# Performance work log

Measured on AMD Instinct MI355X. Metric: run time of the kernel, lower is better.

## Reference

```python
import jax, jax.numpy as jnp
import numpy as np

K = 16          # neighbors
LEAKY = 0.2     # LeakyReLU negative slope
EPS = 1e-5      # BatchNorm eps


def _edge_feature(x, k):
    # x: (B, C, N) -> edge features (B, 2C, N, k)
    xt = jnp.swapaxes(x, 1, 2)                      # (B, N, C)
    sq = jnp.sum(xt * xt, axis=-1)                  # (B, N)
    inner = jnp.einsum('bnc,bmc->bnm', xt, xt)      # (B, N, N)
    # negative squared distance (larger = closer), matches torch topk of -dist
    pd = 2.0 * inner - sq[:, :, None] - sq[:, None, :]
    _, idx = jax.lax.top_k(pd, k)                   # (B, N, k) int32
    # gather neighbors: neigh[b,n,j,c] = xt[b, idx[b,n,j], c]
    neigh = jnp.take_along_axis(xt[:, None, :, :], idx[:, :, :, None], axis=2)  # (B,N,k,C)
    center = jnp.broadcast_to(xt[:, :, None, :], neigh.shape)
    ef = jnp.concatenate([center, neigh - center], axis=-1)  # (B, N, k, 2C)
    return jnp.transpose(ef, (0, 3, 1, 2))                   # (B, 2C, N, k)


def _conv_bn_lrelu_relu(ef, W, gamma, beta):
    # 1x1 conv (no bias) + BatchNorm2d (training-mode batch stats) + LeakyReLU + ReLU
    y = jnp.einsum('oc,bcnk->bonk', W, ef)          # (B, O, N, k)
    mean = jnp.mean(y, axis=(0, 2, 3), keepdims=True)
    var = jnp.mean(jnp.square(y - mean), axis=(0, 2, 3), keepdims=True)
    y = (y - mean) * jax.lax.rsqrt(var + EPS)
    y = gamma[None, :, None, None] * y + beta[None, :, None, None]
    y = jnp.where(y > 0, y, LEAKY * y)              # LeakyReLU(0.2)
    return jax.nn.relu(y)                           # outer F.relu in forward


def setup_inputs() -> dict:
    key = jax.random.key(0)
    ks = jax.random.split(key, 12)
    B, C, N = 8, 3, 4096
    d = {
        'x':   jax.random.normal(ks[0], (B, C, N), jnp.float32),
        'W1':  jax.random.normal(ks[1], (32, 6), jnp.float32) * (1.0 / np.sqrt(6)),
        'g1':  jnp.ones((32,), jnp.float32),
        'b1':  jnp.zeros((32,), jnp.float32),
        'W2':  jax.random.normal(ks[2], (32, 64), jnp.float32) * (1.0 / np.sqrt(64)),
        'g2':  jnp.ones((32,), jnp.float32),
        'b2':  jnp.zeros((32,), jnp.float32),
        'W3':  jax.random.normal(ks[3], (64, 64), jnp.float32) * (1.0 / np.sqrt(64)),
        'g3':  jnp.ones((64,), jnp.float32),
        'b3':  jnp.zeros((64,), jnp.float32),
        'Wfc': jax.random.normal(ks[4], (64, 128), jnp.float32) * (1.0 / np.sqrt(128)),
        'bfc': jnp.zeros((64,), jnp.float32),
    }
    return d


def reference(x, W1, g1, b1, W2, g2, b2, W3, g3, b3, Wfc, bfc):
    x1 = jnp.max(_conv_bn_lrelu_relu(_edge_feature(x,  K), W1, g1, b1), axis=-1)  # (B,32,N)
    x2 = jnp.max(_conv_bn_lrelu_relu(_edge_feature(x1, K), W2, g2, b2), axis=-1)  # (B,32,N)
    x3 = jnp.max(_conv_bn_lrelu_relu(_edge_feature(x2, K), W3, g3, b3), axis=-1)  # (B,64,N)
    x_cat = jnp.concatenate([x1, x2, x3], axis=1)   # (B, 128, N)
    x_global = jnp.max(x_cat, axis=-1)              # (B, 128)
    return x_global @ Wfc.T + bfc                   # (B, 64)
```

## Files before the change

kernel.cpp:

```cpp
#include <hip/hip_runtime.h>

constexpr int B_ = 8;
constexpr int N_ = 4096;
constexpr int BN_ = B_ * N_;
constexpr float BN_EPS = 1e-5f;
constexpr int NCH_ = 8;

__global__ void prep0_kernel(const float* __restrict__ x, float* __restrict__ xa0) {
  int i = blockIdx.x * 256 + threadIdx.x;
  int b = i >> 12, n = i & (N_ - 1);
  const float* xb = x + (size_t)b * 3 * N_;
  float x0 = xb[n], x1 = xb[N_ + n], x2 = xb[2 * N_ + n];
  float4 v = make_float4(x0, x1, x2, -0.5f * (x0 * x0 + x1 * x1 + x2 * x2));
  *reinterpret_cast<float4*>(xa0 + (size_t)i * 4) = v;
}

__device__ __forceinline__ float min16f(const float tv[16]) {
  float m0 = fminf(tv[0], tv[1]),   m1 = fminf(tv[2], tv[3]);
  float m2 = fminf(tv[4], tv[5]),   m3 = fminf(tv[6], tv[7]);
  float m4 = fminf(tv[8], tv[9]),   m5 = fminf(tv[10], tv[11]);
  float m6 = fminf(tv[12], tv[13]), m7 = fminf(tv[14], tv[15]);
  return fminf(fminf(fminf(m0, m1), fminf(m2, m3)), fminf(fminf(m4, m5), fminf(m6, m7)));
}

__device__ __forceinline__ void replace16(float tv[16], int ti[16], float d, int idx,
                                          float& curmin) {
  unsigned mp = __float_as_uint(curmin);
  unsigned s = mp & 15u;
  float dp = __uint_as_float((__float_as_uint(d) & ~15u) | s);
#pragma unroll
  for (int k = 0; k < 16; ++k) {
    bool hit = (__float_as_uint(tv[k]) == mp);
    tv[k] = hit ? dp : tv[k];
    ti[k] = hit ? idx : ti[k];
  }
  curmin = min16f(tv);
}

template<int CQ>
__global__ __launch_bounds__(256, 4) void knn_kernel(const float* __restrict__ xa,
                                                     float2* __restrict__ cand16) {
  constexpr int STR = CQ * 4;
  constexpr int NF = (CQ == 1) ? 3 : 32;
  constexpr int TILE = 128;
  constexpr int CHUNK = 4096 / NCH_;
  constexpr int NT = CHUNK / TILE;
  constexpr int TILE_F = TILE * STR;
  constexpr int NPRE = (TILE_F / 4 + 255) / 256;
  __shared__ float tile[2][TILE_F];

  const int b = blockIdx.y;
  const int chunk = blockIdx.x & (NCH_ - 1);
  const int rg = blockIdx.x / NCH_;
  const int row = rg * 256 + threadIdx.x;
  const float* base = xa + (size_t)b * N_ * STR;

  float rf[NF];
  if constexpr (CQ == 1) {
    float4 v = *reinterpret_cast<const float4*>(base + (size_t)row * STR);
    rf[0] = v.x; rf[1] = v.y; rf[2] = v.z;
  } else {
#pragma unroll
    for (int q = 0; q < 8; ++q) {
      float4 v = *reinterpret_cast<const float4*>(base + (size_t)row * STR + 4 * q);
      rf[4 * q] = v.x; rf[4 * q + 1] = v.y; rf[4 * q + 2] = v.z; rf[4 * q + 3] = v.w;
    }
  }

  float tv[16]; int ti[16];
#pragma unroll
  for (int i = 0; i < 16; ++i) {
    tv[i] = __uint_as_float((__float_as_uint(-3.0e38f) & ~15u) | (unsigned)i);
    ti[i] = 0;
  }
  float curmin = min16f(tv);

  const int m0 = chunk * CHUNK;

  {
    const float4* src = reinterpret_cast<const float4*>(base + (size_t)m0 * STR);
    float4* dst = reinterpret_cast<float4*>(tile[0]);
    for (int f = threadIdx.x; f < TILE_F / 4; f += 256) dst[f] = src[f];
  }
  __syncthreads();

  for (int t = 0; t < NT; ++t) {
    const int cur = t & 1;
    float4 pre[NPRE];
    const bool hasNext = (t + 1 < NT);
    if (hasNext) {
      const float4* src = reinterpret_cast<const float4*>(base + (size_t)(m0 + (t + 1) * TILE) * STR);
#pragma unroll
      for (int k = 0; k < NPRE; ++k) {
        int f = threadIdx.x + k * 256;
        if (f < TILE_F / 4) pre[k] = src[f];
      }
    }
    const float* tl = tile[cur];
    for (int mb = 0; mb < TILE; mb += 8) {
      float d[8];
#pragma unroll
      for (int q8 = 0; q8 < 8; ++q8) {
        const float* cf = tl + (mb + q8) * STR;
        float a;
        if constexpr (CQ == 1) {
          float4 v = *reinterpret_cast<const float4*>(cf);
          a = v.w;
          a = fmaf(rf[0], v.x, a);
          a = fmaf(rf[1], v.y, a);
          a = fmaf(rf[2], v.z, a);
        } else {
          a = cf[32];
#pragma unroll
          for (int q = 0; q < 8; ++q) {
            float4 v = reinterpret_cast<const float4*>(cf)[q];
            a = fmaf(rf[4 * q], v.x, a);
            a = fmaf(rf[4 * q + 1], v.y, a);
            a = fmaf(rf[4 * q + 2], v.z, a);
            a = fmaf(rf[4 * q + 3], v.w, a);
          }
        }
        d[q8] = a;
      }
      float mx = d[0];
#pragma unroll
      for (int q8 = 1; q8 < 8; ++q8) mx = fmaxf(mx, d[q8]);
      const int mbase = m0 + t * TILE + mb;
      if (mx > curmin) {
#pragma unroll
        for (int q8 = 0; q8 < 8; ++q8)
          if (d[q8] > curmin) replace16(tv, ti, d[q8], mbase + q8, curmin);
      }
    }
    if (hasNext) {
      float4* dst = reinterpret_cast<float4*>(tile[cur ^ 1]);
#pragma unroll
      for (int k = 0; k < NPRE; ++k) {
        int f = threadIdx.x + k * 256;
        if (f < TILE_F / 4) dst[f] = pre[k];
      }
    }
    __syncthreads();
  }

  float2* outp = cand16 + ((size_t)(chunk * B_ + b) * N_ + row) * 16;
#pragma unroll
  for (int i = 0; i < 16; ++i)
    outp[i] = make_float2(tv[i], __int_as_float(ti[i]));
}

__global__ void knn_merge_kernel(const float2* __restrict__ cand16, int* __restrict__ idx_out) {
  const int i = blockIdx.x * 256 + threadIdx.x;
  float tv[16]; int ti[16];
  const float2* c0 = cand16 + (size_t)i * 16;
#pragma unroll
  for (int k = 0; k < 16; ++k) { float2 pr = c0[k]; tv[k] = pr.x; ti[k] = __float_as_int(pr.y); }
  float curmin = min16f(tv);
  for (int c = 1; c < NCH_; ++c) {
    const float2* cc = cand16 + ((size_t)c * BN_ + i) * 16;
#pragma unroll
    for (int k = 0; k < 16; ++k) {
      float2 pr = cc[k];
      if (pr.x > curmin) replace16(tv, ti, pr.x, __float_as_int(pr.y), curmin);
    }
  }
  int4* op = reinterpret_cast<int4*>(idx_out + (size_t)i * 16);
  op[0] = make_int4(ti[0], ti[1], ti[2], ti[3]);
  op[1] = make_int4(ti[4], ti[5], ti[6], ti[7]);
  op[2] = make_int4(ti[8], ti[9], ti[10], ti[11]);
  op[3] = make_int4(ti[12], ti[13], ti[14], ti[15]);
}

template<int CIN, int O, int ASTR>
__global__ __launch_bounds__(256) void conv_kernel(const float* __restrict__ xa,
                                                   const int* __restrict__ idxg,
                                                   const float* __restrict__ W,
                                                   float* __restrict__ ymax, float* __restrict__ ymin,
                                                   float* __restrict__ partial) {
  constexpr int PPB = 32;
  constexpr int JPL = (O == 64) ? 16 : 8;
  __shared__ float Wt[2 * CIN * O];
  __shared__ float dbuf[4][CIN * 16];
  __shared__ float ls1[O], ls2[O];

  const int tid = threadIdx.x;
  const int lane = tid & 63;
  const int wv = tid >> 6;

  for (int i = tid; i < 2 * CIN * O; i += 256) {
    int c = i / O, o2 = i % O;
    Wt[i] = W[o2 * (2 * CIN) + c];
  }
  if (tid < O) { ls1[tid] = 0.f; ls2[tid] = 0.f; }
  __syncthreads();

  const int o = lane % O;
  const int jh = lane / O;
  const int j0 = jh * JPL;
  const int j = lane & 15;
  const int cg = lane >> 4;

  float wreg[CIN];
#pragma unroll
  for (int c = 0; c < CIN; ++c) wreg[c] = Wt[(CIN + c) * O + o];

  float s1 = 0.f, s2 = 0.f;
  float* dw = dbuf[wv];

  const int pbase = blockIdx.x * PPB + wv * (PPB / 4);
  for (int p = pbase; p < pbase + PPB / 4; ++p) {
    const int b = p >> 12;
    const float* cp = xa + (size_t)p * ASTR;
    float cf[CIN];
    if constexpr (CIN == 3) {
      float4 v = *reinterpret_cast<const float4*>(cp);
      cf[0] = v.x; cf[1] = v.y; cf[2] = v.z;
    } else {
#pragma unroll
      for (int q = 0; q < CIN / 4; ++q) {
        float4 v = *reinterpret_cast<const float4*>(cp + 4 * q);
        cf[4 * q] = v.x; cf[4 * q + 1] = v.y; cf[4 * q + 2] = v.z; cf[4 * q + 3] = v.w;
      }
    }
    const int idxj = idxg[(size_t)p * 16 + j];
    const float* np = xa + (size_t)(b * N_ + idxj) * ASTR;
    if constexpr (CIN == 3) {
      if (cg == 0) {
        float4 nv = *reinterpret_cast<const float4*>(np);
        dw[0 * 16 + j] = nv.x - cf[0];
        dw[1 * 16 + j] = nv.y - cf[1];
        dw[2 * 16 + j] = nv.z - cf[2];
      }
    } else {
      float4 na = *reinterpret_cast<const float4*>(np + cg * 8);
      float4 nb2 = *reinterpret_cast<const float4*>(np + cg * 8 + 4);
      float4 ca = *reinterpret_cast<const float4*>(cp + cg * 8);
      float4 cb = *reinterpret_cast<const float4*>(cp + cg * 8 + 4);
      dw[(cg * 8 + 0) * 16 + j] = na.x - ca.x;
      dw[(cg * 8 + 1) * 16 + j] = na.y - ca.y;
      dw[(cg * 8 + 2) * 16 + j] = na.z - ca.z;
      dw[(cg * 8 + 3) * 16 + j] = na.w - ca.w;
      dw[(cg * 8 + 4) * 16 + j] = nb2.x - cb.x;
      dw[(cg * 8 + 5) * 16 + j] = nb2.y - cb.y;
      dw[(cg * 8 + 6) * 16 + j] = nb2.z - cb.z;
      dw[(cg * 8 + 7) * 16 + j] = nb2.w - cb.w;
    }
    float y0 = 0.f;
#pragma unroll
    for (int c = 0; c < CIN; ++c) y0 = fmaf(Wt[c * O + o], cf[c], y0);
    float y[JPL];
#pragma unroll
    for (int jj = 0; jj < JPL; ++jj) y[jj] = y0;
#pragma unroll
    for (int c = 0; c < CIN; ++c) {
      float w = wreg[c];
#pragma unroll
      for (int jq = 0; jq < JPL / 4; ++jq) {
        float4 d4 = *reinterpret_cast<const float4*>(dw + c * 16 + j0 + 4 * jq);
        y[4 * jq + 0] = fmaf(w, d4.x, y[4 * jq + 0]);
        y[4 * jq + 1] = fmaf(w, d4.y, y[4 * jq + 1]);
        y[4 * jq + 2] = fmaf(w, d4.z, y[4 * jq + 2]);
        y[4 * jq + 3] = fmaf(w, d4.w, y[4 * jq + 3]);
      }
    }
    float mx = y[0], mn = y[0];
#pragma unroll
    for (int jj = 0; jj < JPL; ++jj) {
      s1 += y[jj];
      s2 = fmaf(y[jj], y[jj], s2);
      if (jj) { mx = fmaxf(mx, y[jj]); mn = fminf(mn, y[jj]); }
    }
    if constexpr (O == 32) {
      mx = fmaxf(mx, __shfl_xor(mx, 32));
      mn = fminf(mn, __shfl_xor(mn, 32));
    }
    ymax[(size_t)p * O + o] = mx;
    ymin[(size_t)p * O + o] = mn;
  }
  atomicAdd(&ls1[o], s1);
  atomicAdd(&ls2[o], s2);
  __syncthreads();
  if (tid < O) {
    partial[(size_t)blockIdx.x * (2 * O) + tid] = ls1[tid];
    partial[(size_t)blockIdx.x * (2 * O) + O + tid] = ls2[tid];
  }
}

template<int O>
__global__ void bnprep_kernel(const float* __restrict__ partial,
                              const float* __restrict__ gamma, const float* __restrict__ beta,
                              float* __restrict__ ab) {
  __shared__ float r1[256], r2[256];
  const int o = blockIdx.x;
  float a1 = 0.f, a2 = 0.f;
  for (int i = threadIdx.x; i < 1024; i += 256) {
    a1 += partial[(size_t)i * (2 * O) + o];
    a2 += partial[(size_t)i * (2 * O) + O + o];
  }
  r1[threadIdx.x] = a1; r2[threadIdx.x] = a2;
  __syncthreads();
  for (int s = 128; s > 0; s >>= 1) {
    if (threadIdx.x < s) { r1[threadIdx.x] += r1[threadIdx.x + s]; r2[threadIdx.x] += r2[threadIdx.x + s]; }
    __syncthreads();
  }
  if (threadIdx.x == 0) {
    const double cnt = (double)BN_ * 16.0;
    double mean = (double)r1[0] / cnt;
    double var = (double)r2[0] / cnt - mean * mean;
    double a = (double)gamma[o] / sqrt(var + (double)BN_EPS);
    ab[o] = (float)a;
    ab[64 + o] = (float)((double)beta[o] - mean * a);
  }
}

template<int O, bool WRITE_XA, int GOFF>
__global__ __launch_bounds__(256) void finalize_kernel(const float* __restrict__ ymax,
                                                       const float* __restrict__ ymin,
                                                       const float* __restrict__ ab,
                                                       float* __restrict__ xa_out,
                                                       float* __restrict__ gmax) {
  __shared__ float la[O], lb[O];
  __shared__ unsigned lgm[O];
  const int tid = threadIdx.x;
  if (tid < O) { la[tid] = ab[tid]; lb[tid] = ab[64 + tid]; lgm[tid] = 0u; }
  __syncthreads();
  const int p = blockIdx.x * 256 + tid;
  const int b = p >> 12;
  float sq = 0.f;
#pragma unroll
  for (int q = 0; q < O / 4; ++q) {
    float4 mx = *reinterpret_cast<const float4*>(ymax + (size_t)p * O + 4 * q);
    float4 mn = *reinterpret_cast<const float4*>(ymin + (size_t)p * O + 4 * q);
    float r0, r1, r2, r3;
    { float a = la[4*q+0], c = lb[4*q+0]; r0 = fmaxf(fmaf(a, (a > 0.f ? mx.x : mn.x), c), 0.f); }
    { float a = la[4*q+1], c = lb[4*q+1]; r1 = fmaxf(fmaf(a, (a > 0.f ? mx.y : mn.y), c), 0.f); }
    { float a = la[4*q+2], c = lb[4*q+2]; r2 = fmaxf(fmaf(a, (a > 0.f ? mx.z : mn.z), c), 0.f); }
    { float a = la[4*q+3], c = lb[4*q+3]; r3 = fmaxf(fmaf(a, (a > 0.f ? mx.w : mn.w), c), 0.f); }
    sq = fmaf(r0, r0, sq); sq = fmaf(r1, r1, sq); sq = fmaf(r2, r2, sq); sq = fmaf(r3, r3, sq);
    atomicMax(&lgm[4*q+0], __float_as_uint(r0));
    atomicMax(&lgm[4*q+1], __float_as_uint(r1));
    atomicMax(&lgm[4*q+2], __float_as_uint(r2));
    atomicMax(&lgm[4*q+3], __float_as_uint(r3));
    if constexpr (WRITE_XA)
      *reinterpret_cast<float4*>(xa_out + (size_t)p * 36 + 4 * q) = make_float4(r0, r1, r2, r3);
  }
  if constexpr (WRITE_XA) {
    xa_out[(size_t)p * 36 + 32] = -0.5f * sq;
    xa_out[(size_t)p * 36 + 33] = 0.f;
    xa_out[(size_t)p * 36 + 34] = 0.f;
    xa_out[(size_t)p * 36 + 35] = 0.f;
  }
  __syncthreads();
  if (tid < O)
    atomicMax(reinterpret_cast<unsigned*>(gmax) + b * 128 + GOFF + tid, lgm[tid]);
}

__global__ void fc_kernel(const float* __restrict__ gmax, const float* __restrict__ Wfc,
                          const float* __restrict__ bfc, float* __restrict__ outp) {
  const int t = blockIdx.x * 256 + threadIdx.x;
  const int b = t >> 6, o = t & 63;
  float acc = bfc[o];
  const float* g = gmax + b * 128;
  const float* w = Wfc + o * 128;
#pragma unroll
  for (int c = 0; c < 128; ++c) acc = fmaf(g[c], w[c], acc);
  outp[(size_t)b * 64 + o] = acc;
}

extern "C" void kernel_launch(void* const* d_in, const int* in_sizes, int n_in,
                              void* d_out, int out_size, void* d_ws, size_t ws_size,
                              hipStream_t stream) {
  (void)in_sizes; (void)n_in; (void)out_size; (void)ws_size;
  const float* x   = (const float*)d_in[0];
  const float* W1  = (const float*)d_in[1];
  const float* g1  = (const float*)d_in[2];
  const float* b1  = (const float*)d_in[3];
  const float* W2  = (const float*)d_in[4];
  const float* g2  = (const float*)d_in[5];
  const float* b2  = (const float*)d_in[6];
  const float* W3  = (const float*)d_in[7];
  const float* g3  = (const float*)d_in[8];
  const float* b3  = (const float*)d_in[9];
  const float* Wfc = (const float*)d_in[10];
  const float* bfc = (const float*)d_in[11];
  float* outp = (float*)d_out;

  char* ws = (char*)d_ws;
  size_t off = 0;
  auto alloc = [&](size_t bytes) { char* p = ws + off; off += (bytes + 511) & ~(size_t)511; return p; };
  float* gmax    = (float*)alloc((size_t)B_ * 128 * 4);
  float* ab      = (float*)alloc(128 * 4);
  float* xa0     = (float*)alloc((size_t)BN_ * 4 * 4);
  float* xa1     = (float*)alloc((size_t)BN_ * 36 * 4);
  float* xa2     = (float*)alloc((size_t)BN_ * 36 * 4);
  int*   idxb    = (int*)  alloc((size_t)BN_ * 16 * 4);
  char*  uni     = alloc((size_t)NCH_ * BN_ * 16 * 8);
  float2* cand16 = (float2*)uni;
  float* ymax    = (float*)uni;
  float* ymin    = (float*)(uni + (size_t)BN_ * 64 * 4);
  float* partial = (float*)(uni + (size_t)BN_ * 64 * 8);

  hipMemsetAsync(gmax, 0, (size_t)B_ * 128 * 4, stream);

  dim3 blk(256);
  prep0_kernel<<<BN_ / 256, blk, 0, stream>>>(x, xa0);

  knn_kernel<1><<<dim3(16 * NCH_, 8), blk, 0, stream>>>(xa0, cand16);
  knn_merge_kernel<<<BN_ / 256, blk, 0, stream>>>(cand16, idxb);
  conv_kernel<3, 32, 4><<<BN_ / 32, blk, 0, stream>>>(xa0, idxb, W1, ymax, ymin, partial);
  bnprep_kernel<32><<<32, blk, 0, stream>>>(partial, g1, b1, ab);
  finalize_kernel<32, true, 0><<<BN_ / 256, blk, 0, stream>>>(ymax, ymin, ab, xa1, gmax);

  knn_kernel<9><<<dim3(16 * NCH_, 8), blk, 0, stream>>>(xa1, cand16);
  knn_merge_kernel<<<BN_ / 256, blk, 0, stream>>>(cand16, idxb);
  conv_kernel<32, 32, 36><<<BN_ / 32, blk, 0, stream>>>(xa1, idxb, W2, ymax, ymin, partial);
  bnprep_kernel<32><<<32, blk, 0, stream>>>(partial, g2, b2, ab);
  finalize_kernel<32, true, 32><<<BN_ / 256, blk, 0, stream>>>(ymax, ymin, ab, xa2, gmax);

  knn_kernel<9><<<dim3(16 * NCH_, 8), blk, 0, stream>>>(xa2, cand16);
  knn_merge_kernel<<<BN_ / 256, blk, 0, stream>>>(cand16, idxb);
  conv_kernel<32, 64, 36><<<BN_ / 32, blk, 0, stream>>>(xa2, idxb, W3, ymax, ymin, partial);
  bnprep_kernel<64><<<64, blk, 0, stream>>>(partial, g3, b3, ab);
  finalize_kernel<64, false, 64><<<BN_ / 256, blk, 0, stream>>>(ymax, ymin, ab, nullptr, gmax);

  fc_kernel<<<2, blk, 0, stream>>>(gmax, Wfc, bfc, outp);
}
```

Measured before the change: 1.537 ms.

## Replace LDS candidate tiles with register buffers broadcast via readlane

The kNN kernel no longer stages candidate points through double-buffered shared memory with block barriers. Each wave now loads 64 candidates into registers, one per lane, and broadcasts each candidate's features to all lanes with readlane, ping-ponging between two register buffers. This removes LDS traffic and __syncthreads. The cost is one extra VALU readlane per feature per candidate and more register pressure, so the occupancy hint drops from 4 to 3 blocks.

```diff
diff --git a/kernel.cpp b/kernel.cpp
--- a/kernel.cpp
+++ b/kernel.cpp
@@ -37,22 +37,21 @@
   curmin = min16f(tv);
 }
 
+__device__ __forceinline__ float rl(float v, int l) {
+  return __int_as_float(__builtin_amdgcn_readlane(__float_as_int(v), l));
+}
+
 template<int CQ>
-__global__ __launch_bounds__(256, 4) void knn_kernel(const float* __restrict__ xa,
+__global__ __launch_bounds__(256, 3) void knn_kernel(const float* __restrict__ xa,
                                                      float2* __restrict__ cand16) {
   constexpr int STR = CQ * 4;
   constexpr int NF = (CQ == 1) ? 3 : 32;
-  constexpr int TILE = 128;
   constexpr int CHUNK = 4096 / NCH_;
-  constexpr int NT = CHUNK / TILE;
-  constexpr int TILE_F = TILE * STR;
-  constexpr int NPRE = (TILE_F / 4 + 255) / 256;
-  __shared__ float tile[2][TILE_F];
-
   const int b = blockIdx.y;
   const int chunk = blockIdx.x & (NCH_ - 1);
   const int rg = blockIdx.x / NCH_;
   const int row = rg * 256 + threadIdx.x;
+  const int lane = threadIdx.x & 63;
   const float* base = xa + (size_t)b * N_ * STR;
 
   float rf[NF];
@@ -77,70 +76,55 @@
 
   const int m0 = chunk * CHUNK;
 
-  {
-    const float4* src = reinterpret_cast<const float4*>(base + (size_t)m0 * STR);
-    float4* dst = reinterpret_cast<float4*>(tile[0]);
-    for (int f = threadIdx.x; f < TILE_F / 4; f += 256) dst[f] = src[f];
-  }
-  __syncthreads();
-
-  for (int t = 0; t < NT; ++t) {
-    const int cur = t & 1;
-    float4 pre[NPRE];
-    const bool hasNext = (t + 1 < NT);
-    if (hasNext) {
-      const float4* src = reinterpret_cast<const float4*>(base + (size_t)(m0 + (t + 1) * TILE) * STR);
-#pragma unroll
-      for (int k = 0; k < NPRE; ++k) {
-        int f = threadIdx.x + k * 256;
-        if (f < TILE_F / 4) pre[k] = src[f];
-      }
-    }
-    const float* tl = tile[cur];
-    for (int mb = 0; mb < TILE; mb += 8) {
+  float4 bufA[CQ], bufB[CQ];
+
+  auto loadblk = [&](float4 (&dst)[CQ], int cb) {
+    const float4* src = reinterpret_cast<const float4*>(base + (size_t)(m0 + cb + lane) * STR);
+#pragma unroll
+    for (int q = 0; q < CQ; ++q) dst[q] = src[q];
+  };
+
+  auto process = [&](float4 (&cbuf)[CQ], int mb0) {
+    for (int g = 0; g < 64; g += 8) {
       float d[8];
 #pragma unroll
-      for (int q8 = 0; q8 < 8; ++q8) {
-        const float* cf = tl + (mb + q8) * STR;
+      for (int jj = 0; jj < 8; ++jj) {
+        const int j = g + jj;
         float a;
         if constexpr (CQ == 1) {
-          float4 v = *reinterpret_cast<const float4*>(cf);
-          a = v.w;
-          a = fmaf(rf[0], v.x, a);
-          a = fmaf(rf[1], v.y, a);
-          a = fmaf(rf[2], v.z, a);
+          a = rl(cbuf[0].w, j);
+          a = fmaf(rf[0], rl(cbuf[0].x, j), a);
+          a = fmaf(rf[1], rl(cbuf[0].y, j), a);
+          a = fmaf(rf[2], rl(cbuf[0].z, j), a);
         } else {
-          a = cf[32];
+          a = rl(cbuf[8].x, j);
 #pragma unroll
           for (int q = 0; q < 8; ++q) {
-            float4 v = reinterpret_cast<const float4*>(cf)[q];
-            a = fmaf(rf[4 * q], v.x, a);
-            a = fmaf(rf[4 * q + 1], v.y, a);
-            a = fmaf(rf[4 * q + 2], v.z, a);
-            a = fmaf(rf[4 * q + 3], v.w, a);
+            a = fmaf(rf[4 * q + 0], rl(cbuf[q].x, j), a);
+            a = fmaf(rf[4 * q + 1], rl(cbuf[q].y, j), a);
+            a = fmaf(rf[4 * q + 2], rl(cbuf[q].z, j), a);
+            a = fmaf(rf[4 * q + 3], rl(cbuf[q].w, j), a);
           }
         }
-        d[q8] = a;
+        d[jj] = a;
       }
       float mx = d[0];
 #pragma unroll
-      for (int q8 = 1; q8 < 8; ++q8) mx = fmaxf(mx, d[q8]);
-      const int mbase = m0 + t * TILE + mb;
+      for (int jj = 1; jj < 8; ++jj) mx = fmaxf(mx, d[jj]);
       if (mx > curmin) {
 #pragma unroll
-        for (int q8 = 0; q8 < 8; ++q8)
-          if (d[q8] > curmin) replace16(tv, ti, d[q8], mbase + q8, curmin);
+        for (int jj = 0; jj < 8; ++jj)
+          if (d[jj] > curmin) replace16(tv, ti, d[jj], mb0 + g + jj, curmin);
       }
     }
-    if (hasNext) {
-      float4* dst = reinterpret_cast<float4*>(tile[cur ^ 1]);
-#pragma unroll
-      for (int k = 0; k < NPRE; ++k) {
-        int f = threadIdx.x + k * 256;
-        if (f < TILE_F / 4) dst[f] = pre[k];
-      }
-    }
-    __syncthreads();
+  };
+
+  loadblk(bufA, 0);
+  for (int cb = 0; cb < CHUNK; cb += 128) {
+    loadblk(bufB, cb + 64);
+    process(bufA, m0 + cb);
+    if (cb + 128 < CHUNK) loadblk(bufA, cb + 128);
+    process(bufB, m0 + cb + 64);
   }
 
   float2* outp = cand16 + ((size_t)(chunk * B_ + b) * N_ + row) * 16;
```

After: 2.102 ms. 1.37x slower.
